# Kernel tuning notes

Hardware: AMD Instinct MI355X
Metric: run time of the kernel (lower is better)

The kernel has to match this reference:

```python
import jax, jax.numpy as jnp
import numpy as np

N = 100000   # nodes
E = 640000   # edges (before self-loops)
G = 1000     # graphs in batch
D_IN = 100
D = 128
EPS = 1e-5


def setup_inputs() -> dict:
    key = jax.random.key(0)
    ks = jax.random.split(key, 12)
    x = jax.random.normal(ks[0], (N, D_IN), dtype=jnp.float32)
    edge_index = jax.random.randint(ks[1], (2, E), 0, N, dtype=jnp.int64)
    edge_weight = jax.random.uniform(ks[2], (E,), dtype=jnp.float32)
    batch = jnp.sort(jax.random.randint(ks[3], (N,), 0, G, dtype=jnp.int64))
    def glorot(k, shape):
        fan = shape[0]
        return jax.random.normal(k, shape, dtype=jnp.float32) / np.float32(np.sqrt(fan))
    return {
        "x": x, "edge_index": edge_index, "edge_weight": edge_weight, "batch": batch,
        "W0": glorot(ks[4], (D_IN, D)), "b0": jnp.zeros((D,), jnp.float32),
        "W1": glorot(ks[5], (D, D)),    "b1": jnp.zeros((D,), jnp.float32),
        "W2": glorot(ks[6], (D, D)),    "b2": jnp.zeros((D,), jnp.float32),
        "gamma": jnp.ones((3, D), jnp.float32), "beta": jnp.zeros((3, D), jnp.float32),
        "run_mean": jnp.zeros((3, D), jnp.float32), "run_var": jnp.ones((3, D), jnp.float32),
        "Wout": glorot(ks[7], (D, 1)), "bout": jnp.zeros((1,), jnp.float32),
    }


def reference(x, edge_index, edge_weight, batch, W0, b0, W1, b1, W2, b2,
              gamma, beta, run_mean, run_var, Wout, bout):
    n = x.shape[0]
    # add self-loops with weight 1 (GCNConv default)
    loop = jnp.arange(n, dtype=edge_index.dtype)
    src = jnp.concatenate([edge_index[0], loop])
    dst = jnp.concatenate([edge_index[1], loop])
    ew = jnp.concatenate([edge_weight, jnp.ones((n,), edge_weight.dtype)])
    # symmetric normalization: D^{-1/2} A D^{-1/2}
    deg = jax.ops.segment_sum(ew, dst, num_segments=n)
    dinv = jnp.where(deg > 0, jax.lax.rsqrt(deg), 0.0)
    norm = dinv[src] * ew * dinv[dst]            # [E+N]

    def gcn_bn_relu(h, W, b, g, bt, rm, rv):
        h = h @ W                                 # linear first (cheaper gather dim)
        agg = jax.ops.segment_sum(h[src] * norm[:, None], dst, num_segments=n)
        agg = agg + b
        # BatchNorm1d in eval mode (running stats); dropout is identity in eval
        agg = g * (agg - rm) * jax.lax.rsqrt(rv + EPS) + bt
        return jax.nn.relu(agg)

    h = gcn_bn_relu(x, W0, b0, gamma[0], beta[0], run_mean[0], run_var[0])
    h = gcn_bn_relu(h, W1, b1, gamma[1], beta[1], run_mean[1], run_var[1])
    h = gcn_bn_relu(h, W2, b2, gamma[2], beta[2], run_mean[2], run_var[2])

    # global mean pool over graphs
    counts = jax.ops.segment_sum(jnp.ones((n,), h.dtype), batch, num_segments=G)
    pooled = jax.ops.segment_sum(h, batch, num_segments=G) / jnp.maximum(counts, 1.0)[:, None]
    return pooled @ Wout + bout
```

## Files before the change

### kernel.cpp

```cpp
#include <hip/hip_runtime.h>

#define BN_EPS 1e-5f
#define BINCAP 32

static inline size_t align_up(size_t x, size_t a) { return (x + a - 1) & ~(a - 1); }

typedef __attribute__((ext_vector_type(8))) short bf16x8;
typedef __attribute__((ext_vector_type(4))) float f32x4;

__device__ __forceinline__ void bf16split(float v, unsigned short& hi, unsigned short& lo) {
    unsigned u = __float_as_uint(v);
    unsigned rh = (u + 0x7FFFu + ((u >> 16) & 1u)) >> 16;
    float fh = __uint_as_float(rh << 16);
    hi = (unsigned short)rh;
    float rem = v - fh;
    unsigned u2 = __float_as_uint(rem);
    lo = (unsigned short)((u2 + 0x7FFFu + ((u2 >> 16) & 1u)) >> 16);
}

__device__ __forceinline__ unsigned short bf16rne(float v) {
    unsigned u = __float_as_uint(v);
    return (unsigned short)((u + 0x7FFFu + ((u >> 16) & 1u)) >> 16);
}

__device__ __forceinline__ float bf16f(unsigned h) { return __uint_as_float(h << 16); }
__device__ __forceinline__ float chlo(unsigned u) { return __uint_as_float(u << 16); }
__device__ __forceinline__ float chhi(unsigned u) { return __uint_as_float(u & 0xffff0000u); }


__global__ void place_kernel(const int* __restrict__ src, const int* __restrict__ dst,
                             const float* __restrict__ ew,
                             int* __restrict__ cntc, int2* __restrict__ bins, int E) {
    int e = blockIdx.x * blockDim.x + threadIdx.x;
    if (e >= E) return;
    int d = dst[e];
    int pos = atomicAdd(&cntc[d], 1);
    if (pos < BINCAP)
        bins[(size_t)d * BINCAP + pos] = make_int2(src[e], __float_as_int(ew[e]));
}


__global__ void deginv_kernel(const int* __restrict__ cntc, const int2* __restrict__ bins,
                              float* __restrict__ dinv, int N) {
    int i = blockIdx.x * blockDim.x + threadIdx.x;
    if (i >= N) return;
    int cnt = cntc[i]; if (cnt > BINCAP) cnt = BINCAP;
    const int2* b = bins + (size_t)i * BINCAP;
    float s = 0.f;
    for (int j = 0; j < cnt; ++j) s += __int_as_float(b[j].y);
    dinv[i] = rsqrtf(s + 1.0f);
}


__global__ void normfix_kernel(const int* __restrict__ cntc, int2* __restrict__ bins,
                               const float* __restrict__ dinv, int N) {
    int i = blockIdx.x * blockDim.x + threadIdx.x;
    if (i >= N) return;
    int cnt = cntc[i]; if (cnt > BINCAP) cnt = BINCAP;
    float di = dinv[i];
    int2* b = bins + (size_t)i * BINCAP;
    for (int j = 0; j < cnt; ++j) {
        int2 pr = b[j];
        float w = __int_as_float(pr.y) * dinv[pr.x] * di;
        b[j].y = __float_as_int(w);
    }
}


__global__ void prep_kernel(const float* __restrict__ W0, const float* __restrict__ W1,
                            const float* __restrict__ W2, int K0,
                            unsigned short* __restrict__ Whi, unsigned short* __restrict__ Wlo,
                            const float* __restrict__ gamma, const float* __restrict__ beta,
                            const float* __restrict__ rm, const float* __restrict__ rv,
                            const float* __restrict__ b0, const float* __restrict__ b1,
                            const float* __restrict__ b2,
                            float* __restrict__ scale, float* __restrict__ shift,
                            const int* __restrict__ batch, int* __restrict__ gstart,
                            int N, int G) {
    int idx = blockIdx.x * blockDim.x + threadIdx.x;
    if (idx < 3 * 32 * 64 * 8) {
        int j    = idx & 7;
        int lane = (idx >> 3) & 63;
        int f    = (idx >> 9) & 31;
        int l    = idx >> 14;
        int ct = f >> 2, k0c = f & 3;
        int quad = lane >> 4, m16 = lane & 15;
        int n = ct * 16 + m16;
        int k = k0c * 32 + quad * 8 + j;
        const float* W = (l == 0) ? W0 : (l == 1) ? W1 : W2;
        int Kl = (l == 0) ? K0 : 128;
        float v = (k < Kl) ? W[(size_t)k * 128 + n] : 0.f;
        unsigned short hi, lo;
        bf16split(v, hi, lo);
        Whi[idx] = hi;
        Wlo[idx] = lo;
    } else if (idx < 3 * 32 * 64 * 8 + 384) {
        int t = idx - 3 * 32 * 64 * 8;
        int l = t >> 7, j = t & 127;
        const float* bs = (l == 0) ? b0 : (l == 1) ? b1 : b2;
        float sc = gamma[t] * rsqrtf(rv[t] + BN_EPS);
        scale[t] = sc;
        shift[t] = beta[t] + (bs[j] - rm[t]) * sc;
    } else {
        int i = idx - (3 * 32 * 64 * 8 + 384);
        if (i >= N) return;
        int b = batch[i];
        int prev = (i == 0) ? -1 : batch[i - 1];
        for (int g = prev + 1; g <= b; ++g) gstart[g] = i;
        if (i == N - 1) {
            for (int g = b + 1; g <= G; ++g) gstart[g] = N;
        }
    }
}


__device__ __forceinline__ void mfma_tail(const bf16x8 ah[4], const bf16x8 al[4],
                                          const unsigned short* __restrict__ Whi,
                                          const unsigned short* __restrict__ Wlo,
                                          unsigned short* __restrict__ Yh,
                                          int row0, int quad, int m16, int lane, int N) {
    const bf16x8* Wh8 = (const bf16x8*)Whi;
    const bf16x8* Wl8 = (const bf16x8*)Wlo;

    f32x4 acc[8];
    #pragma unroll
    for (int ct = 0; ct < 8; ++ct) acc[ct] = (f32x4){0.f, 0.f, 0.f, 0.f};

    bf16x8 bh[2][4], bl[2][4];
    #pragma unroll
    for (int k0c = 0; k0c < 4; ++k0c) {
        bh[0][k0c] = Wh8[k0c * 64 + lane];
        bl[0][k0c] = Wl8[k0c * 64 + lane];
    }

    __builtin_amdgcn_s_setprio(1);
    #pragma unroll
    for (int ct = 0; ct < 8; ++ct) {
        int cur = ct & 1, nxt = cur ^ 1;
        if (ct < 7) {
            #pragma unroll
            for (int k0c = 0; k0c < 4; ++k0c) {
                bh[nxt][k0c] = Wh8[((ct + 1) * 4 + k0c) * 64 + lane];
                bl[nxt][k0c] = Wl8[((ct + 1) * 4 + k0c) * 64 + lane];
            }
        }
        #pragma unroll
        for (int k0c = 0; k0c < 4; ++k0c) {
            acc[ct] = __builtin_amdgcn_mfma_f32_16x16x32_bf16(ah[k0c], bh[cur][k0c], acc[ct], 0, 0, 0);
            acc[ct] = __builtin_amdgcn_mfma_f32_16x16x32_bf16(ah[k0c], bl[cur][k0c], acc[ct], 0, 0, 0);
            acc[ct] = __builtin_amdgcn_mfma_f32_16x16x32_bf16(al[k0c], bh[cur][k0c], acc[ct], 0, 0, 0);
        }
    }
    __builtin_amdgcn_s_setprio(0);

    #pragma unroll
    for (int ct = 0; ct < 8; ++ct) {
        #pragma unroll
        for (int rg = 0; rg < 4; ++rg) {
            int row = row0 + quad * 4 + rg;
            if (row < N)
                Yh[(size_t)row * 128 + ct * 16 + m16] = bf16rne(acc[ct][rg]);
        }
    }
}


__launch_bounds__(256, 2)
__global__ void gemm0_fused_kernel(const float* __restrict__ x, int D_IN,
                                   const unsigned short* __restrict__ Whi,
                                   const unsigned short* __restrict__ Wlo,
                                   unsigned short* __restrict__ Yh, int N) {
    int tid = threadIdx.x;
    int wid = tid >> 6, lane = tid & 63;
    int quad = lane >> 4, m16 = lane & 15;
    int row0 = blockIdx.x * 64 + wid * 16;

    int arow = row0 + m16;
    if (arow > N - 1) arow = N - 1;
    const float* xr = x + (size_t)arow * D_IN;

    bf16x8 ah[4], al[4];
    #pragma unroll
    for (int k0c = 0; k0c < 4; ++k0c) {
        int kb = k0c * 32 + quad * 8;
        float vs[8];
        if (kb + 8 <= D_IN) {
            float4 v0 = *((const float4*)(xr + kb));
            float4 v1 = *((const float4*)(xr + kb + 4));
            vs[0] = v0.x; vs[1] = v0.y; vs[2] = v0.z; vs[3] = v0.w;
            vs[4] = v1.x; vs[5] = v1.y; vs[6] = v1.z; vs[7] = v1.w;
        } else {
            #pragma unroll
            for (int j = 0; j < 8; ++j) vs[j] = (kb + j < D_IN) ? xr[kb + j] : 0.f;
        }
        #pragma unroll
        for (int j = 0; j < 8; ++j) {
            unsigned short hi, lo;
            bf16split(vs[j], hi, lo);
            ah[k0c][j] = (short)hi;
            al[k0c][j] = (short)lo;
        }
    }

    mfma_tail(ah, al, Whi, Wlo, Yh, row0, quad, m16, lane, N);
}


__device__ __forceinline__ void gather_quad(const unsigned* __restrict__ Yh32,
                                            const int2* pr, const int* mq, int lane,
                                            float* ax, float* ay) {
    int mr = mq[0];
    if (mq[1] > mr) mr = mq[1];
    if (mq[2] > mr) mr = mq[2];
    if (mq[3] > mr) mr = mq[3];
    mr = (mr + 7) & ~7;
    for (int j = 0; j < mr; j += 8) {
        unsigned u[4][8];
        #pragma unroll
        for (int q = 0; q < 4; ++q) {
            #pragma unroll
            for (int t = 0; t < 8; ++t) {
                int s = __builtin_amdgcn_readlane(pr[q].x, j + t);
                u[q][t] = Yh32[(size_t)s * 64 + lane];
            }
        }
        #pragma unroll
        for (int q = 0; q < 4; ++q) {
            #pragma unroll
            for (int t = 0; t < 8; ++t) {
                float w = __int_as_float(__builtin_amdgcn_readlane(pr[q].y, j + t));
                ax[q] += chlo(u[q][t]) * w;
                ay[q] += chhi(u[q][t]) * w;
            }
        }
    }
}


__launch_bounds__(64, 4)
__global__ void fused_agg_gemm_kernel(
        const unsigned* __restrict__ Yh_in,
        const int2* __restrict__ bins, const int* __restrict__ cntc,
        const float* __restrict__ dinv,
        const float* __restrict__ scale, const float* __restrict__ shift,
        const unsigned short* __restrict__ Whi, const unsigned short* __restrict__ Wlo,
        unsigned short* __restrict__ Yh_out, int N) {
    __shared__ float sA[16 * 132];
    int lane = threadIdx.x;
    int quad = lane >> 4, m16 = lane & 15;
    int row0 = blockIdx.x * 16;

    float2 sc = ((const float2*)scale)[lane];
    float2 sh = ((const float2*)shift)[lane];

    int mm[16]; float dv[16]; unsigned uh[16];
    #pragma unroll
    for (int i = 0; i < 16; ++i) {
        int n = row0 + i; if (n > N - 1) n = N - 1;
        mm[i] = cntc[n];
        dv[i] = dinv[n];
        uh[i] = Yh_in[(size_t)n * 64 + lane];
    }
    #pragma unroll
    for (int i = 0; i < 16; ++i) { int m = mm[i]; if (m > BINCAP) m = BINCAP; mm[i] = m; }

    int2 gq[2][4];
    #pragma unroll
    for (int q = 0; q < 4; ++q) {
        int n = row0 + q; if (n > N - 1) n = N - 1;
        gq[0][q] = (lane < mm[q]) ? bins[(size_t)n * BINCAP + lane] : make_int2(n, 0);
    }

    #pragma unroll
    for (int b = 0; b < 4; ++b) {
        int cur = b & 1, nxt = cur ^ 1;
        if (b < 3) {
            #pragma unroll
            for (int q = 0; q < 4; ++q) {
                int i = (b + 1) * 4 + q;
                int n = row0 + i; if (n > N - 1) n = N - 1;
                gq[nxt][q] = (lane < mm[i]) ? bins[(size_t)n * BINCAP + lane] : make_int2(n, 0);
            }
        }
        float ax[4], ay[4];
        #pragma unroll
        for (int q = 0; q < 4; ++q) {
            float w0 = dv[b * 4 + q] * dv[b * 4 + q];
            ax[q] = chlo(uh[b * 4 + q]) * w0;
            ay[q] = chhi(uh[b * 4 + q]) * w0;
        }
        gather_quad(Yh_in, gq[cur], &mm[b * 4], lane, ax, ay);
        #pragma unroll
        for (int q = 0; q < 4; ++q) {
            float ox = fmaxf(ax[q] * sc.x + sh.x, 0.f);
            float oy = fmaxf(ay[q] * sc.y + sh.y, 0.f);
            *((float2*)&sA[(b * 4 + q) * 132 + 2 * lane]) = make_float2(ox, oy);
        }
    }

    asm volatile("s_waitcnt lgkmcnt(0)" ::: "memory");
    __builtin_amdgcn_sched_barrier(0);

    bf16x8 ah[4], al[4];
    #pragma unroll
    for (int k0c = 0; k0c < 4; ++k0c) {
        float4 v0 = *((const float4*)&sA[m16 * 132 + k0c * 32 + quad * 8]);
        float4 v1 = *((const float4*)&sA[m16 * 132 + k0c * 32 + quad * 8 + 4]);
        float vs[8] = {v0.x, v0.y, v0.z, v0.w, v1.x, v1.y, v1.z, v1.w};
        #pragma unroll
        for (int j = 0; j < 8; ++j) {
            unsigned short hi, lo;
            bf16split(vs[j], hi, lo);
            ah[k0c][j] = (short)hi;
            al[k0c][j] = (short)lo;
        }
    }

    mfma_tail(ah, al, Whi, Wlo, Yh_out, row0, quad, m16, lane, N);
}


__launch_bounds__(256)
__global__ void agg3_kernel(const unsigned* __restrict__ Yh32,
                            const int2* __restrict__ bins, const int* __restrict__ cntc,
                            const float* __restrict__ dinv,
                            const float* __restrict__ scale, const float* __restrict__ shift,
                            const float* __restrict__ Wout,
                            float* __restrict__ snode, int N) {
    int idx = blockIdx.x * blockDim.x + threadIdx.x;
    int waveid = idx >> 6, lane = idx & 63;
    int n0 = waveid * 4;
    if (n0 >= N) return;

    int nn[4]; int mq[4]; float dvq[4]; unsigned uhq[4]; int2 gg[4];
    #pragma unroll
    for (int q = 0; q < 4; ++q) {
        int n = n0 + q; if (n > N - 1) n = N - 1;
        nn[q] = n;
        mq[q] = cntc[n];
        dvq[q] = dinv[n];
        uhq[q] = Yh32[(size_t)n * 64 + lane];
    }
    #pragma unroll
    for (int q = 0; q < 4; ++q) {
        int m = mq[q]; if (m > BINCAP) m = BINCAP;
        mq[q] = m;
        gg[q] = (lane < m) ? bins[(size_t)nn[q] * BINCAP + lane] : make_int2(nn[q], 0);
    }

    float ax[4], ay[4];
    #pragma unroll
    for (int q = 0; q < 4; ++q) {
        float w0 = dvq[q] * dvq[q];
        ax[q] = chlo(uhq[q]) * w0;
        ay[q] = chhi(uhq[q]) * w0;
    }
    gather_quad(Yh32, gg, mq, lane, ax, ay);

    float2 sc = ((const float2*)scale)[lane];
    float2 sh = ((const float2*)shift)[lane];
    float2 w  = ((const float2*)Wout)[lane];
    float s[4];
    #pragma unroll
    for (int q = 0; q < 4; ++q) {
        float ox = fmaxf(ax[q] * sc.x + sh.x, 0.f);
        float oy = fmaxf(ay[q] * sc.y + sh.y, 0.f);
        s[q] = ox * w.x + oy * w.y;
    }
    #pragma unroll
    for (int off = 32; off > 0; off >>= 1) {
        #pragma unroll
        for (int q = 0; q < 4; ++q) s[q] += __shfl_down(s[q], off, 64);
    }
    if (lane == 0) {
        #pragma unroll
        for (int q = 0; q < 4; ++q)
            if (n0 + q < N) snode[n0 + q] = s[q];
    }
}


__launch_bounds__(256)
__global__ void pool3_kernel(const float* __restrict__ snode, const int* __restrict__ gstart,
                             const float* __restrict__ bout, float* __restrict__ out, int G) {
    int g = blockIdx.x;
    int beg = gstart[g], end = gstart[g + 1];
    int t = threadIdx.x;
    float acc = 0.f;
    for (int n = beg + t; n < end; n += 256) acc += snode[n];
    __shared__ float lds[256];
    lds[t] = acc;
    __syncthreads();
    if (t < 64) lds[t] = lds[t] + lds[t + 64] + lds[t + 128] + lds[t + 192];
    __syncthreads();
    if (t < 64) {
        float s = lds[t];
        #pragma unroll
        for (int off = 32; off > 0; off >>= 1) s += __shfl_down(s, off, 64);
        if (t == 0) {
            float cntf = (float)(end - beg);
            out[g] = s / fmaxf(cntf, 1.0f) + bout[0];
        }
    }
}


extern "C" void kernel_launch(void* const* d_in, const int* in_sizes, int n_in,
                              void* d_out, int out_size, void* d_ws, size_t ws_size,
                              hipStream_t stream) {
    const float* x     = (const float*)d_in[0];
    const int*   ei    = (const int*)d_in[1];
    const float* ew    = (const float*)d_in[2];
    const int*   batch = (const int*)d_in[3];
    const float* W0 = (const float*)d_in[4];
    const float* b0 = (const float*)d_in[5];
    const float* W1 = (const float*)d_in[6];
    const float* b1 = (const float*)d_in[7];
    const float* W2 = (const float*)d_in[8];
    const float* b2 = (const float*)d_in[9];
    const float* gamma = (const float*)d_in[10];
    const float* beta  = (const float*)d_in[11];
    const float* rmean = (const float*)d_in[12];
    const float* rvar  = (const float*)d_in[13];
    const float* Wout  = (const float*)d_in[14];
    const float* bout  = (const float*)d_in[15];

    const int E = in_sizes[2];
    const int N = in_sizes[3];
    const int D_IN = in_sizes[0] / N;
    const int G = out_size;

    const int* src = ei;
    const int* dst = ei + E;

    char* ws = (char*)d_ws;
    size_t off = 0;
    float* dinv  = (float*)(ws + off); off = align_up(off + (size_t)N * 4, 256);
    int* cntc    = (int*)(ws + off);   off = align_up(off + (size_t)N * 4, 256);
    int* gstart  = (int*)(ws + off);   off = align_up(off + ((size_t)G + 1) * 4, 256);
    int2* bins   = (int2*)(ws + off);  off = align_up(off + (size_t)N * BINCAP * 8, 256);
    unsigned short* YAh = (unsigned short*)(ws + off); off = align_up(off + (size_t)N * 128 * 2, 256);
    unsigned short* YBh = (unsigned short*)(ws + off); off = align_up(off + (size_t)N * 128 * 2, 256);
    unsigned short* Whi = (unsigned short*)(ws + off); off = align_up(off + 3 * 16384 * 2, 256);
    unsigned short* Wlo = (unsigned short*)(ws + off); off = align_up(off + 3 * 16384 * 2, 256);
    float* scale = (float*)(ws + off); off = align_up(off + 3 * 128 * 4, 256);
    float* shift = (float*)(ws + off); off = align_up(off + 3 * 128 * 4, 256);
    float* snode = (float*)(ws + off); off = align_up(off + (size_t)N * 4, 256);
    (void)ws_size;

    hipMemsetAsync(cntc, 0, (size_t)N * 4, stream);

    const int tB = 256;
    place_kernel<<<(E + tB - 1) / tB, tB, 0, stream>>>(src, dst, ew, cntc, bins, E);
    deginv_kernel<<<(N + tB - 1) / tB, tB, 0, stream>>>(cntc, bins, dinv, N);
    normfix_kernel<<<(N + tB - 1) / tB, tB, 0, stream>>>(cntc, bins, dinv, N);
    {
        int prep_threads = 3 * 32 * 64 * 8 + 384 + N;
        prep_kernel<<<(prep_threads + tB - 1) / tB, tB, 0, stream>>>(
            W0, W1, W2, D_IN, Whi, Wlo,
            gamma, beta, rmean, rvar, b0, b1, b2, scale, shift,
            batch, gstart, N, G);
    }

    int gemm0_blocks = (N + 63) / 64;
    int fused_blocks = (N + 15) / 16;

    gemm0_fused_kernel<<<gemm0_blocks, 256, 0, stream>>>(x, D_IN, Whi, Wlo, YAh, N);
    fused_agg_gemm_kernel<<<fused_blocks, 64, 0, stream>>>(
        (const unsigned*)YAh, bins, cntc, dinv,
        scale, shift, Whi + 16384, Wlo + 16384, YBh, N);
    fused_agg_gemm_kernel<<<fused_blocks, 64, 0, stream>>>(
        (const unsigned*)YBh, bins, cntc, dinv,
        scale + 128, shift + 128, Whi + 2 * 16384, Wlo + 2 * 16384, YAh, N);
    {
        long nthread_quad = (long)((N + 3) / 4) * 64;
        int blocks_quad = (int)((nthread_quad + tB - 1) / tB);
        agg3_kernel<<<blocks_quad, tB, 0, stream>>>((const unsigned*)YAh,
            bins, cntc, dinv, scale + 256, shift + 256, Wout, snode, N);
    }

    pool3_kernel<<<G, 256, 0, stream>>>(snode, gstart, bout, (float*)d_out, G);
}
```

Baseline: 320.8 us.

## Sort nodes by in-degree so aggregation wavefronts process balanced rows

Builds a histogram of per-node in-degree, scans it, and produces a node permutation grouped by degree. The aggregation kernels then process nodes in this order, so the 16 or 4 nodes handled together have similar edge counts and lanes diverge less. Outputs are scattered back to the original node rows. The cost is extra kernels with contended atomics on a 33-entry histogram, plus less locality on row reads and writes.

```diff
diff --git a/kernel.cpp b/kernel.cpp
--- a/kernel.cpp
+++ b/kernel.cpp
@@ -23,7 +23,6 @@
     return (unsigned short)((u + 0x7FFFu + ((u >> 16) & 1u)) >> 16);
 }
 
-__device__ __forceinline__ float bf16f(unsigned h) { return __uint_as_float(h << 16); }
 __device__ __forceinline__ float chlo(unsigned u) { return __uint_as_float(u << 16); }
 __device__ __forceinline__ float chhi(unsigned u) { return __uint_as_float(u & 0xffff0000u); }
 
@@ -41,7 +40,7 @@
 
 
 __global__ void deginv_kernel(const int* __restrict__ cntc, const int2* __restrict__ bins,
-                              float* __restrict__ dinv, int N) {
+                              float* __restrict__ dinv, int* __restrict__ hist, int N) {
     int i = blockIdx.x * blockDim.x + threadIdx.x;
     if (i >= N) return;
     int cnt = cntc[i]; if (cnt > BINCAP) cnt = BINCAP;
@@ -49,11 +48,21 @@
     float s = 0.f;
     for (int j = 0; j < cnt; ++j) s += __int_as_float(b[j].y);
     dinv[i] = rsqrtf(s + 1.0f);
+    atomicAdd(&hist[cnt], 1);
+}
+
+
+__global__ void scan_kernel(int* __restrict__ hist) {
+    if (threadIdx.x == 0) {
+        int run = 0;
+        for (int c = 0; c <= BINCAP; ++c) { int h = hist[c]; hist[c] = run; run += h; }
+    }
 }
 
 
 __global__ void normfix_kernel(const int* __restrict__ cntc, int2* __restrict__ bins,
-                               const float* __restrict__ dinv, int N) {
+                               const float* __restrict__ dinv,
+                               int* __restrict__ offs, int* __restrict__ order, int N) {
     int i = blockIdx.x * blockDim.x + threadIdx.x;
     if (i >= N) return;
     int cnt = cntc[i]; if (cnt > BINCAP) cnt = BINCAP;
@@ -64,6 +73,8 @@
         float w = __int_as_float(pr.y) * dinv[pr.x] * di;
         b[j].y = __float_as_int(w);
     }
+    int pos = atomicAdd(&offs[cnt], 1);
+    order[pos] = i;
 }
 
 
@@ -118,7 +129,8 @@
                                           const unsigned short* __restrict__ Whi,
                                           const unsigned short* __restrict__ Wlo,
                                           unsigned short* __restrict__ Yh,
-                                          int row0, int quad, int m16, int lane, int N) {
+                                          const int* ord16, int row0,
+                                          int quad, int m16, int lane, int N) {
     const bf16x8* Wh8 = (const bf16x8*)Whi;
     const bf16x8* Wl8 = (const bf16x8*)Wlo;
 
@@ -157,9 +169,9 @@
     for (int ct = 0; ct < 8; ++ct) {
         #pragma unroll
         for (int rg = 0; rg < 4; ++rg) {
-            int row = row0 + quad * 4 + rg;
-            if (row < N)
-                Yh[(size_t)row * 128 + ct * 16 + m16] = bf16rne(acc[ct][rg]);
+            int slot = quad * 4 + rg;
+            if (row0 + slot < N)
+                Yh[(size_t)ord16[slot] * 128 + ct * 16 + m16] = bf16rne(acc[ct][rg]);
         }
     }
 }
@@ -202,7 +214,11 @@
         }
     }
 
-    mfma_tail(ah, al, Whi, Wlo, Yh, row0, quad, m16, lane, N);
+    int ord16[16];
+    #pragma unroll
+    for (int i = 0; i < 16; ++i) ord16[i] = row0 + i;
+
+    mfma_tail(ah, al, Whi, Wlo, Yh, ord16, row0, quad, m16, lane, N);
 }
 
 
@@ -241,7 +257,7 @@
 __global__ void fused_agg_gemm_kernel(
         const unsigned* __restrict__ Yh_in,
         const int2* __restrict__ bins, const int* __restrict__ cntc,
-        const float* __restrict__ dinv,
+        const float* __restrict__ dinv, const int* __restrict__ order,
         const float* __restrict__ scale, const float* __restrict__ shift,
         const unsigned short* __restrict__ Whi, const unsigned short* __restrict__ Wlo,
         unsigned short* __restrict__ Yh_out, int N) {
@@ -253,10 +269,17 @@
     float2 sc = ((const float2*)scale)[lane];
     float2 sh = ((const float2*)shift)[lane];
 
+    int ord[16];
+    #pragma unroll
+    for (int i = 0; i < 16; ++i) {
+        int slot = row0 + i; if (slot > N - 1) slot = N - 1;
+        ord[i] = order[slot];
+    }
+
     int mm[16]; float dv[16]; unsigned uh[16];
     #pragma unroll
     for (int i = 0; i < 16; ++i) {
-        int n = row0 + i; if (n > N - 1) n = N - 1;
+        int n = ord[i];
         mm[i] = cntc[n];
         dv[i] = dinv[n];
         uh[i] = Yh_in[(size_t)n * 64 + lane];
@@ -267,7 +290,7 @@
     int2 gq[2][4];
     #pragma unroll
     for (int q = 0; q < 4; ++q) {
-        int n = row0 + q; if (n > N - 1) n = N - 1;
+        int n = ord[q];
         gq[0][q] = (lane < mm[q]) ? bins[(size_t)n * BINCAP + lane] : make_int2(n, 0);
     }
 
@@ -278,7 +301,7 @@
             #pragma unroll
             for (int q = 0; q < 4; ++q) {
                 int i = (b + 1) * 4 + q;
-                int n = row0 + i; if (n > N - 1) n = N - 1;
+                int n = ord[i];
                 gq[nxt][q] = (lane < mm[i]) ? bins[(size_t)n * BINCAP + lane] : make_int2(n, 0);
             }
         }
@@ -316,14 +339,14 @@
         }
     }
 
-    mfma_tail(ah, al, Whi, Wlo, Yh_out, row0, quad, m16, lane, N);
+    mfma_tail(ah, al, Whi, Wlo, Yh_out, ord, row0, quad, m16, lane, N);
 }
 
 
 __launch_bounds__(256)
 __global__ void agg3_kernel(const unsigned* __restrict__ Yh32,
                             const int2* __restrict__ bins, const int* __restrict__ cntc,
-                            const float* __restrict__ dinv,
+                            const float* __restrict__ dinv, const int* __restrict__ order,
                             const float* __restrict__ scale, const float* __restrict__ shift,
                             const float* __restrict__ Wout,
                             float* __restrict__ snode, int N) {
@@ -335,7 +358,8 @@
     int nn[4]; int mq[4]; float dvq[4]; unsigned uhq[4]; int2 gg[4];
     #pragma unroll
     for (int q = 0; q < 4; ++q) {
-        int n = n0 + q; if (n > N - 1) n = N - 1;
+        int slot = n0 + q; if (slot > N - 1) slot = N - 1;
+        int n = order[slot];
         nn[q] = n;
         mq[q] = cntc[n];
         dvq[q] = dinv[n];
@@ -375,7 +399,7 @@
     if (lane == 0) {
         #pragma unroll
         for (int q = 0; q < 4; ++q)
-            if (n0 + q < N) snode[n0 + q] = s[q];
+            if (n0 + q < N) snode[nn[q]] = s[q];
     }
 }
 
@@ -437,6 +461,8 @@
     size_t off = 0;
     float* dinv  = (float*)(ws + off); off = align_up(off + (size_t)N * 4, 256);
     int* cntc    = (int*)(ws + off);   off = align_up(off + (size_t)N * 4, 256);
+    int* hist    = (int*)(ws + off);   off = align_up(off + (BINCAP + 1) * 4, 256);
+    int* order   = (int*)(ws + off);   off = align_up(off + (size_t)N * 4, 256);
     int* gstart  = (int*)(ws + off);   off = align_up(off + ((size_t)G + 1) * 4, 256);
     int2* bins   = (int2*)(ws + off);  off = align_up(off + (size_t)N * BINCAP * 8, 256);
     unsigned short* YAh = (unsigned short*)(ws + off); off = align_up(off + (size_t)N * 128 * 2, 256);
@@ -449,11 +475,13 @@
     (void)ws_size;
 
     hipMemsetAsync(cntc, 0, (size_t)N * 4, stream);
+    hipMemsetAsync(hist, 0, (BINCAP + 1) * 4, stream);
 
     const int tB = 256;
     place_kernel<<<(E + tB - 1) / tB, tB, 0, stream>>>(src, dst, ew, cntc, bins, E);
-    deginv_kernel<<<(N + tB - 1) / tB, tB, 0, stream>>>(cntc, bins, dinv, N);
-    normfix_kernel<<<(N + tB - 1) / tB, tB, 0, stream>>>(cntc, bins, dinv, N);
+    deginv_kernel<<<(N + tB - 1) / tB, tB, 0, stream>>>(cntc, bins, dinv, hist, N);
+    scan_kernel<<<1, 64, 0, stream>>>(hist);
+    normfix_kernel<<<(N + tB - 1) / tB, tB, 0, stream>>>(cntc, bins, dinv, hist, order, N);
     {
         int prep_threads = 3 * 32 * 64 * 8 + 384 + N;
         prep_kernel<<<(prep_threads + tB - 1) / tB, tB, 0, stream>>>(
@@ -467,16 +495,16 @@
 
     gemm0_fused_kernel<<<gemm0_blocks, 256, 0, stream>>>(x, D_IN, Whi, Wlo, YAh, N);
     fused_agg_gemm_kernel<<<fused_blocks, 64, 0, stream>>>(
-        (const unsigned*)YAh, bins, cntc, dinv,
+        (const unsigned*)YAh, bins, cntc, dinv, order,
         scale, shift, Whi + 16384, Wlo + 16384, YBh, N);
     fused_agg_gemm_kernel<<<fused_blocks, 64, 0, stream>>>(
-        (const unsigned*)YBh, bins, cntc, dinv,
+        (const unsigned*)YBh, bins, cntc, dinv, order,
         scale + 128, shift + 128, Whi + 2 * 16384, Wlo + 2 * 16384, YAh, N);
     {
         long nthread_quad = (long)((N + 3) / 4) * 64;
         int blocks_quad = (int)((nthread_quad + tB - 1) / tB);
         agg3_kernel<<<blocks_quad, tB, 0, stream>>>((const unsigned*)YAh,
-            bins, cntc, dinv, scale + 256, shift + 256, Wout, snode, N);
+            bins, cntc, dinv, order, scale + 256, shift + 256, Wout, snode, N);
     }
 
     pool3_kernel<<<G, 256, 0, stream>>>(snode, gstart, bout, (float*)d_out, G);
```

New measurement: 1.074 ms. +234.9%, slower.
